# Kernel tuning notes

Hardware: AMD Instinct MI355X
Metric: run time of the kernel (lower is better)

## Reference

```python
import jax, jax.numpy as jnp
import numpy as np

T, H, I, E, Z = 1024, 2048, 1024, 8, 8  # tokens, hidden, moe_intermediate, routed experts, zero experts
TOP_K = 4
ROUTED_SCALING = 1.0


def setup_inputs() -> dict:
    key = jax.random.key(0)
    k0, k1, k2, k3, k4 = jax.random.split(key, 5)
    s = 0.02
    return {
        "hidden_states": jax.random.normal(k0, (T, H), dtype=jnp.float32),
        "router_w": jax.random.normal(k1, (E + Z, H), dtype=jnp.float32) * s,   # classifier weight
        "corr_bias": jnp.zeros((E + Z,), dtype=jnp.float32),                     # e_score_correction_bias
        "w_gate": jax.random.normal(k2, (E, H, I), dtype=jnp.float32) * s,
        "w_up": jax.random.normal(k3, (E, H, I), dtype=jnp.float32) * s,
        "w_down": jax.random.normal(k4, (E, I, H), dtype=jnp.float32) * s,
    }


def reference(hidden_states, router_w, corr_bias, w_gate, w_up, w_down):
    x = hidden_states  # [T, H]
    # ---- router (float32) ----
    logits = x.astype(jnp.float32) @ router_w.T                 # [T, E+Z]
    scores = jax.nn.softmax(logits, axis=-1)
    sel_scores = scores + corr_bias                             # bias used for selection only
    _, topk_idx = jax.lax.top_k(sel_scores, TOP_K)              # [T, K]
    topk_w = jnp.take_along_axis(scores, topk_idx, axis=-1)     # gating weights (renormalize=False)
    topk_w = topk_w * ROUTED_SCALING

    routed = topk_idx < E                                       # [T, K] real-expert mask
    # dense combine weights per routed expert: [T, E]
    onehot = jax.nn.one_hot(jnp.where(routed, topk_idx, 0), E, dtype=x.dtype)
    route_w = jnp.einsum("tke,tk->te", onehot, topk_w * routed.astype(x.dtype))

    # ---- routed experts: silu-gated MLP per expert ----
    gate = jnp.einsum("th,ehi->eti", x, w_gate)                 # [E, T, I]
    up = jnp.einsum("th,ehi->eti", x, w_up)
    mid = jax.nn.silu(gate) * up
    down = jnp.einsum("eti,eih->eth", mid, w_down)              # [E, T, H]
    out = jnp.einsum("te,eth->th", route_w, down)               # combine

    # ---- zero experts (identity type): weight * hidden_states ----
    zero_w = jnp.sum(topk_w * (~routed).astype(x.dtype), axis=-1)  # [T]
    out = out + zero_w[:, None] * x
    return out.astype(hidden_states.dtype)
```

## Files before the change

kernel.cpp:

```cpp
#include <hip/hip_runtime.h>
#include <hip/hip_bf16.h>
#include <math.h>

constexpr int T   = 1024;
constexpr int H   = 2048;
constexpr int I   = 1024;
constexpr int E   = 8;
constexpr int NEZ = 16;
constexpr int TK  = 4;
constexpr int MTG = 24;

typedef short bf16x8 __attribute__((ext_vector_type(8)));
typedef float f32x4  __attribute__((ext_vector_type(4)));
typedef unsigned short u16;
typedef u16 u16x8 __attribute__((ext_vector_type(8)));

#define SYNC() do { asm volatile("s_waitcnt lgkmcnt(0)" ::: "memory"); \
                    __builtin_amdgcn_s_barrier(); } while (0)

__device__ __forceinline__ u16 bf16rn(float x) {
  unsigned u = __builtin_bit_cast(unsigned, x);
  u = u + 0x7FFFu + ((u >> 16) & 1u);
  return (u16)(u >> 16);
}
__device__ __forceinline__ float bf16tof(u16 h) {
  return __builtin_bit_cast(float, (unsigned)h << 16);
}

__global__ __launch_bounds__(256) void prep_a_kernel(
    const float* __restrict__ x, const int* __restrict__ cnt,
    const int* __restrict__ list, u16* __restrict__ Axh, u16* __restrict__ Axl)
{
  const int kt = blockIdx.x;
  const int e  = blockIdx.y;
  int ce = cnt[e]; if (ce > MTG * 16) ce = MTG * 16;
  if (ce == 0) return;
  const int tid = threadIdx.x;
  const int w = tid >> 6, lane = tid & 63;
  const int l15 = lane & 15, lg = lane >> 4;

  for (int mtg = w; mtg < MTG; mtg += 4) {
    int r = mtg * 16 + l15; if (r >= ce) r = ce - 1;
    const int tok = list[e * T + r] >> 2;
    const float* src = x + (size_t)tok * H + kt * 32 + lg * 8;
    const float4 v0 = *(const float4*)(src);
    const float4 v1 = *(const float4*)(src + 4);
    const float vv[8] = {v0.x, v0.y, v0.z, v0.w, v1.x, v1.y, v1.z, v1.w};
    u16x8 h8, l8;
#pragma unroll
    for (int j = 0; j < 8; j++) {
      const u16 hh = bf16rn(vv[j]);
      h8[j] = hh;
      l8[j] = bf16rn(vv[j] - bf16tof(hh));
    }
    const size_t off = (((size_t)e * 64 + kt) * MTG + mtg) * 512 + (size_t)lane * 8;
    *(u16x8*)(Axh + off) = h8;
    *(u16x8*)(Axl + off) = l8;
  }
}

__global__ __launch_bounds__(256) void router_kernel(
    const float* __restrict__ x, const float* __restrict__ rw,
    const float* __restrict__ bias, int* __restrict__ cnt,
    int* __restrict__ list, float* __restrict__ wk4,
    float* __restrict__ zerow)
{
  const int t   = blockIdx.x;
  const int tid = threadIdx.x;
  const float* xt = x + (size_t)t * H;

  float acc[NEZ];
#pragma unroll
  for (int e = 0; e < NEZ; e++) acc[e] = 0.f;

  for (int h = tid; h < H; h += 256) {
    const float xv = xt[h];
#pragma unroll
    for (int e = 0; e < NEZ; e++) acc[e] = fmaf(xv, rw[e * H + h], acc[e]);
  }

#pragma unroll
  for (int e = 0; e < NEZ; e++) {
    float v = acc[e];
#pragma unroll
    for (int off = 32; off >= 1; off >>= 1) v += __shfl_down(v, off, 64);
    acc[e] = v;
  }

  __shared__ float red[4][NEZ];
  const int wv = tid >> 6, ln = tid & 63;
  if (ln == 0) {
#pragma unroll
    for (int e = 0; e < NEZ; e++) red[wv][e] = acc[e];
  }
  __syncthreads();

  if (tid == 0) {
    float l[NEZ];
    float mx = -1e30f;
#pragma unroll
    for (int e = 0; e < NEZ; e++) {
      l[e] = red[0][e] + red[1][e] + red[2][e] + red[3][e];
      mx = fmaxf(mx, l[e]);
    }
    float s = 0.f;
#pragma unroll
    for (int e = 0; e < NEZ; e++) { l[e] = expf(l[e] - mx); s += l[e]; }
    const float inv = 1.f / s;
    float sc[NEZ], sel[NEZ];
#pragma unroll
    for (int e = 0; e < NEZ; e++) {
      sc[e]  = l[e] * inv;
      sel[e] = sc[e] + bias[e];
    }
    float zw = 0.f;
#pragma unroll
    for (int k = 0; k < TK; k++) {
      int best = 0; float bv = sel[0];
#pragma unroll
      for (int e = 1; e < NEZ; e++) {
        if (sel[e] > bv) { bv = sel[e]; best = e; }
      }
      sel[best] = -1e30f;
      const float w = sc[best];
      if (best < E) {
        const int pos = atomicAdd(&cnt[best], 1);
        list[best * T + pos] = (t << 2) | k;
        wk4[t * TK + k] = w;
      } else {
        wk4[t * TK + k] = 0.f;
        zw += w;
      }
    }
    zerow[t] = zw;
  }
}

__global__ __launch_bounds__(256) void gateup_kernel(
    const u16* __restrict__ Axh, const u16* __restrict__ Axl,
    const float* __restrict__ wg, const float* __restrict__ wu,
    const int* __restrict__ cnt, const int* __restrict__ list,
    u16* __restrict__ midh, u16* __restrict__ midl)
{
  const int p = blockIdx.x;
  const int L = (p & 7) * 64 + (p >> 3);
  const int e = L >> 6;
  const int rem = L & 63;
  const int nu = rem & 31;
  const int tg = rem >> 5;
  const int n0 = nu * 32;
  int ce = cnt[e]; if (ce > MTG * 16) ce = MTG * 16;
  if (ce == 0) return;
  const int ntiers = (ce + 63) >> 6;
  if (tg == 1 && ntiers <= 4) return;

  __shared__ __align__(16) char ldsB[3][8192];

  const int tid = threadIdx.x;
  const int w = tid >> 6, lane = tid & 63;
  const int l15 = lane & 15, lg = lane >> 4;
  const int tier = tg * 4 + w;
  const bool alive = (tier < ntiers);

  const int mat = tid >> 7;
  const int oct = (tid >> 5) & 3;
  const int nl  = tid & 31;
  const int ntgw = nl >> 4;
  const int Lw   = (nl & 15) | (oct << 4);
  const int foh  = ((mat << 2) | ntgw) * 1024 + Lw * 16;
  const float* wsrc = (mat ? wu : wg) + (size_t)e * H * I +
                      (size_t)(oct * 8) * I + (size_t)(n0 + nl);

  const int mt0 = (tier <= 5) ? tier * 4 : MTG - 4;
  const char* pAh = (const char*)Axh + (((size_t)e * 64) * MTG + mt0) * 1024 + (size_t)lane * 16;
  const char* pAl = (const char*)Axl + (((size_t)e * 64) * MTG + mt0) * 1024 + (size_t)lane * 16;

  f32x4 accg[4][2] = {};
  f32x4 accu[4][2] = {};
  bf16x8 a0[8], a1[8], a2[8];
  float s0[8], s1[8], s2[8];

#define GU_ISSUE(S, KT) do {                                              \
    const float* ps_ = wsrc + (size_t)(KT) * (32 * (size_t)I);            \
    _Pragma("unroll") for (int j = 0; j < 8; j++) S[j] = ps_[(size_t)j * I]; \
  } while (0)

#define GU_ALOAD(A, KT) do {                                              \
    const size_t ka_ = (size_t)(KT) * (MTG * 1024);                       \
    _Pragma("unroll") for (int q = 0; q < 4; q++) {                       \
      A[q]     = *(const bf16x8*)(pAh + ka_ + q * 1024);                  \
      A[4 + q] = *(const bf16x8*)(pAl + ka_ + q * 1024);                  \
    } } while (0)

#define GU_CONVW(S, WB) do {                                              \
    u16x8 h8_, l8_;                                                       \
    _Pragma("unroll") for (int j = 0; j < 8; j++) {                       \
      const u16 hh_ = bf16rn(S[j]);                                       \
      h8_[j] = hh_; l8_[j] = bf16rn(S[j] - bf16tof(hh_)); }               \
    *(u16x8*)(&ldsB[WB][0] + foh) = h8_;                                  \
    *(u16x8*)(&ldsB[WB][0] + foh + 2048) = l8_;                           \
  } while (0)

#define GU_COMP(RB, A) do {                                               \
    const char* bp_ = &ldsB[RB][0];                                       \
    _Pragma("unroll") for (int ntg = 0; ntg < 2; ntg++) {                 \
      const bf16x8 ggh = *(const bf16x8*)(bp_ + ntg * 1024        + lane * 16); \
      const bf16x8 ggl = *(const bf16x8*)(bp_ + ntg * 1024 + 2048 + lane * 16); \
      const bf16x8 guh = *(const bf16x8*)(bp_ + ntg * 1024 + 4096 + lane * 16); \
      const bf16x8 gul = *(const bf16x8*)(bp_ + ntg * 1024 + 6144 + lane * 16); \
      _Pragma("unroll") for (int mi = 0; mi < 4; mi++) {                  \
        accg[mi][ntg] = __builtin_amdgcn_mfma_f32_16x16x32_bf16(A[mi],     ggh, accg[mi][ntg], 0, 0, 0); \
        accg[mi][ntg] = __builtin_amdgcn_mfma_f32_16x16x32_bf16(A[mi],     ggl, accg[mi][ntg], 0, 0, 0); \
        accg[mi][ntg] = __builtin_amdgcn_mfma_f32_16x16x32_bf16(A[4 + mi], ggh, accg[mi][ntg], 0, 0, 0); \
        accu[mi][ntg] = __builtin_amdgcn_mfma_f32_16x16x32_bf16(A[mi],     guh, accu[mi][ntg], 0, 0, 0); \
        accu[mi][ntg] = __builtin_amdgcn_mfma_f32_16x16x32_bf16(A[mi],     gul, accu[mi][ntg], 0, 0, 0); \
        accu[mi][ntg] = __builtin_amdgcn_mfma_f32_16x16x32_bf16(A[4 + mi], guh, accu[mi][ntg], 0, 0, 0); \
      } } } while (0)

#define GU_BODY(K, SI, AU, AN, SC, RB, WB) do {                           \
    const int k_ = (K);                                                   \
    SYNC();                                                               \
    if (k_ + 3 < 64) GU_ISSUE(SI, k_ + 3);                                \
    if (k_ + 1 < 64) GU_ALOAD(AN, k_ + 1);                                \
    if (alive) GU_COMP(RB, AU);                                           \
    if (k_ + 1 < 64) GU_CONVW(SC, WB);                                    \
  } while (0)

  GU_ISSUE(s0, 0); GU_ISSUE(s1, 1); GU_ISSUE(s2, 2);
  GU_ALOAD(a0, 0);
  GU_CONVW(s0, 0);

  for (int kb = 0; kb < 63; kb += 3) {
    GU_BODY(kb,     s0, a0, a1, s1, 0, 1);
    GU_BODY(kb + 1, s1, a1, a2, s2, 1, 2);
    GU_BODY(kb + 2, s2, a2, a0, s0, 2, 0);
  }
  GU_BODY(63, s0, a0, a1, s1, 0, 1);

#undef GU_ISSUE
#undef GU_ALOAD
#undef GU_CONVW
#undef GU_COMP
#undef GU_BODY

#pragma unroll
  for (int mi = 0; mi < 4; mi++) {
#pragma unroll
    for (int rr = 0; rr < 4; rr++) {
      const int m = tier * 64 + mi * 16 + lg * 4 + rr;
      if (m >= ce) continue;
#pragma unroll
      for (int ntg = 0; ntg < 2; ntg++) {
        const int n = n0 + ntg * 16 + l15;
        const float g = accg[mi][ntg][rr];
        const float u = accu[mi][ntg][rr];
        const float mv = (g / (1.f + expf(-g))) * u;
        const u16 hh = bf16rn(mv);
        const size_t off =
            (((size_t)e * 32 + (n >> 5)) * MTG + (m >> 4)) * 512 +
            (size_t)((m & 15) + ((n >> 3) & 3) * 16) * 8 + (n & 7);
        midh[off] = hh;
        midl[off] = bf16rn(mv - bf16tof(hh));
      }
    }
  }
}

__global__ __launch_bounds__(256) void down_kernel(
    const u16* __restrict__ midh, const u16* __restrict__ midl,
    const float* __restrict__ wd,
    const int* __restrict__ cnt, const int* __restrict__ list,
    float* __restrict__ downb)
{
  const int p = blockIdx.x;
  const int L = (p & 7) * 64 + (p >> 3);
  const int e = L >> 6;
  const int rem = L & 63;
  const int nu = rem & 31;
  const int tg = rem >> 5;
  const int n0 = nu * 64;
  int ce = cnt[e]; if (ce > MTG * 16) ce = MTG * 16;
  if (ce == 0) return;
  const int ntiers = (ce + 63) >> 6;
  if (tg == 1 && ntiers <= 4) return;

  __shared__ __align__(16) char ldsB[3][8192];

  const int tid = threadIdx.x;
  const int w = tid >> 6, lane = tid & 63;
  const int l15 = lane & 15, lg = lane >> 4;
  const int tier = tg * 4 + w;
  const bool alive = (tier < ntiers);

  const int oct = tid >> 6;
  const int nl  = tid & 63;
  const int ntgw = nl >> 4;
  const int Lw   = (nl & 15) | (oct << 4);
  const int foh  = ntgw * 1024 + Lw * 16;
  const float* wsrc = wd + (size_t)e * I * H +
                      (size_t)(oct * 8) * H + (size_t)(n0 + nl);

  const int mt0 = (tier <= 5) ? tier * 4 : MTG - 4;
  const char* pAh = (const char*)midh + (((size_t)e * 32) * MTG + mt0) * 1024 + (size_t)lane * 16;
  const char* pAl = (const char*)midl + (((size_t)e * 32) * MTG + mt0) * 1024 + (size_t)lane * 16;

  f32x4 acc[4][4] = {};
  bf16x8 a0[8], a1[8], a2[8];
  float s0[8], s1[8], s2[8];

#define DN_ISSUE(S, KT) do {                                              \
    const float* ps_ = wsrc + (size_t)(KT) * (32 * (size_t)H);            \
    _Pragma("unroll") for (int j = 0; j < 8; j++) S[j] = ps_[(size_t)j * H]; \
  } while (0)

#define DN_ALOAD(A, KT) do {                                              \
    const size_t ka_ = (size_t)(KT) * (MTG * 1024);                       \
    _Pragma("unroll") for (int q = 0; q < 4; q++) {                       \
      A[q]     = *(const bf16x8*)(pAh + ka_ + q * 1024);                  \
      A[4 + q] = *(const bf16x8*)(pAl + ka_ + q * 1024);                  \
    } } while (0)

#define DN_CONVW(S, WB) do {                                              \
    u16x8 h8_, l8_;                                                       \
    _Pragma("unroll") for (int j = 0; j < 8; j++) {                       \
      const u16 hh_ = bf16rn(S[j]);                                       \
      h8_[j] = hh_; l8_[j] = bf16rn(S[j] - bf16tof(hh_)); }               \
    *(u16x8*)(&ldsB[WB][0] + foh) = h8_;                                  \
    *(u16x8*)(&ldsB[WB][0] + foh + 4096) = l8_;                           \
  } while (0)

#define DN_COMP(RB, A) do {                                               \
    const char* bp_ = &ldsB[RB][0];                                       \
    _Pragma("unroll") for (int ntg = 0; ntg < 4; ntg++) {                 \
      const bf16x8 bh = *(const bf16x8*)(bp_ + ntg * 1024        + lane * 16); \
      const bf16x8 bl = *(const bf16x8*)(bp_ + ntg * 1024 + 4096 + lane * 16); \
      _Pragma("unroll") for (int mi = 0; mi < 4; mi++) {                  \
        acc[mi][ntg] = __builtin_amdgcn_mfma_f32_16x16x32_bf16(A[mi],     bh, acc[mi][ntg], 0, 0, 0); \
        acc[mi][ntg] = __builtin_amdgcn_mfma_f32_16x16x32_bf16(A[mi],     bl, acc[mi][ntg], 0, 0, 0); \
        acc[mi][ntg] = __builtin_amdgcn_mfma_f32_16x16x32_bf16(A[4 + mi], bh, acc[mi][ntg], 0, 0, 0); \
      } } } while (0)

#define DN_BODY(K, SI, AU, AN, SC, RB, WB) do {                           \
    const int k_ = (K);                                                   \
    SYNC();                                                               \
    if (k_ + 3 < 32) DN_ISSUE(SI, k_ + 3);                                \
    if (k_ + 1 < 32) DN_ALOAD(AN, k_ + 1);                                \
    if (alive) DN_COMP(RB, AU);                                           \
    if (k_ + 1 < 32) DN_CONVW(SC, WB);                                    \
  } while (0)

  DN_ISSUE(s0, 0); DN_ISSUE(s1, 1); DN_ISSUE(s2, 2);
  DN_ALOAD(a0, 0);
  DN_CONVW(s0, 0);

  for (int kb = 0; kb < 30; kb += 3) {
    DN_BODY(kb,     s0, a0, a1, s1, 0, 1);
    DN_BODY(kb + 1, s1, a1, a2, s2, 1, 2);
    DN_BODY(kb + 2, s2, a2, a0, s0, 2, 0);
  }
  DN_BODY(30, s0, a0, a1, s1, 0, 1);
  DN_BODY(31, s1, a1, a2, s2, 1, 2);

#undef DN_ISSUE
#undef DN_ALOAD
#undef DN_CONVW
#undef DN_COMP
#undef DN_BODY

#pragma unroll
  for (int mi = 0; mi < 4; mi++) {
#pragma unroll
    for (int rr = 0; rr < 4; rr++) {
      const int m = tier * 64 + mi * 16 + lg * 4 + rr;
      if (m >= ce) continue;
      const int ent  = list[e * T + m];
      const int tok  = ent >> 2;
      const int slot = ent & 3;
      float* drow = downb + ((size_t)tok * TK + slot) * H;
#pragma unroll
      for (int ntg = 0; ntg < 4; ntg++) {
        const int n = n0 + ntg * 16 + l15;
        drow[n] = acc[mi][ntg][rr];
      }
    }
  }
}

__global__ __launch_bounds__(256) void combine_kernel(
    const float* __restrict__ x, const float* __restrict__ downb,
    const float* __restrict__ wk4, const float* __restrict__ zerow,
    float* __restrict__ out)
{
  const int idx = blockIdx.x * 256 + threadIdx.x;
  const int t   = idx >> 9;
  const int h   = (idx & 511) * 4;

  const float w0 = wk4[t * TK + 0];
  const float w1 = wk4[t * TK + 1];
  const float w2 = wk4[t * TK + 2];
  const float w3 = wk4[t * TK + 3];
  const float zw = zerow[t];

  const float4 xv = *(const float4*)(x + (size_t)t * H + h);
  const float4 d0 = *(const float4*)(downb + ((size_t)t * TK + 0) * H + h);
  const float4 d1 = *(const float4*)(downb + ((size_t)t * TK + 1) * H + h);
  const float4 d2 = *(const float4*)(downb + ((size_t)t * TK + 2) * H + h);
  const float4 d3 = *(const float4*)(downb + ((size_t)t * TK + 3) * H + h);

  float4 o;
  o.x = w0 * d0.x + w1 * d1.x + w2 * d2.x + w3 * d3.x + zw * xv.x;
  o.y = w0 * d0.y + w1 * d1.y + w2 * d2.y + w3 * d3.y + zw * xv.y;
  o.z = w0 * d0.z + w1 * d1.z + w2 * d2.z + w3 * d3.z + zw * xv.z;
  o.w = w0 * d0.w + w1 * d1.w + w2 * d2.w + w3 * d3.w + zw * xv.w;
  *(float4*)(out + (size_t)t * H + h) = o;
}

extern "C" void kernel_launch(void* const* d_in, const int* in_sizes, int n_in,
                              void* d_out, int out_size, void* d_ws, size_t ws_size,
                              hipStream_t stream) {
  const float* x    = (const float*)d_in[0];
  const float* rw   = (const float*)d_in[1];
  const float* bias = (const float*)d_in[2];
  const float* wg   = (const float*)d_in[3];
  const float* wu   = (const float*)d_in[4];
  const float* wd   = (const float*)d_in[5];
  float* out = (float*)d_out;

  char* ws = (char*)d_ws;
  size_t off = 0;
  auto alloc = [&](size_t bytes) {
    void* p = ws + off;
    off = (off + bytes + 1023) & ~(size_t)1023;
    return p;
  };
  int*   cnt   = (int*)  alloc(E * sizeof(int));
  int*   list  = (int*)  alloc((size_t)E * T * sizeof(int));
  float* wk4   = (float*)alloc((size_t)T * TK * sizeof(float));
  float* zerow = (float*)alloc((size_t)T * sizeof(float));
  const size_t AXSZ = (size_t)E * 64 * MTG * 512;
  u16*   Axh   = (u16*)  alloc(AXSZ * sizeof(u16));
  u16*   Axl   = (u16*)  alloc(AXSZ * sizeof(u16));
  const size_t MIDSZ = (size_t)E * 32 * MTG * 512;
  u16*   midh  = (u16*)  alloc(MIDSZ * sizeof(u16));
  u16*   midl  = (u16*)  alloc(MIDSZ * sizeof(u16));
  float* downb = (float*)alloc((size_t)T * TK * H * sizeof(float));
  (void)ws_size;

  hipMemsetAsync(cnt, 0, E * sizeof(int), stream);

  router_kernel<<<T, 256, 0, stream>>>(x, rw, bias, cnt, list, wk4, zerow);
  prep_a_kernel<<<dim3(64, 8), 256, 0, stream>>>(x, cnt, list, Axh, Axl);

  gateup_kernel<<<512, 256, 0, stream>>>(
      Axh, Axl, wg, wu, cnt, list, midh, midl);

  down_kernel<<<512, 256, 0, stream>>>(
      midh, midl, wd, cnt, list, downb);

  combine_kernel<<<(T * H / 4) / 256, 256, 0, stream>>>(
      x, downb, wk4, zerow, out);
}
```

Before: 199.0 us.

## Split expert GEMMs into 128-thread blocks covering two M-tiers each

Both the gate/up and down kernels drop from 256-thread blocks covering four 64-row tiers to 128-thread blocks covering two tiers. The grids grow from 512 to 768 blocks, so M-tier groups are spread more finely and fewer waves sit idle when an expert has few tokens. Each thread now loads and converts twice as many weight elements per k-step to fill the same LDS tile. The trade-off is that each weight tile is reloaded and split into bf16 hi/lo by more blocks, which adds global weight traffic and conversion work, and each thread holds more registers.

Result: slower. 209.3 us (+5.2%).

```diff
diff --git a/kernel.cpp b/kernel.cpp
--- a/kernel.cpp
+++ b/kernel.cpp
@@ -136,40 +136,37 @@
   }
 }
 
-__global__ __launch_bounds__(256) void gateup_kernel(
+__global__ __launch_bounds__(128) void gateup_kernel(
     const u16* __restrict__ Axh, const u16* __restrict__ Axl,
     const float* __restrict__ wg, const float* __restrict__ wu,
     const int* __restrict__ cnt, const int* __restrict__ list,
     u16* __restrict__ midh, u16* __restrict__ midl)
 {
   const int p = blockIdx.x;
-  const int L = (p & 7) * 64 + (p >> 3);
-  const int e = L >> 6;
-  const int rem = L & 63;
-  const int nu = rem & 31;
-  const int tg = rem >> 5;
+  const int e = p & 7;
+  const int q = p >> 3;
+  const int nu = q / 3, mg = q % 3;
   const int n0 = nu * 32;
   int ce = cnt[e]; if (ce > MTG * 16) ce = MTG * 16;
   if (ce == 0) return;
   const int ntiers = (ce + 63) >> 6;
-  if (tg == 1 && ntiers <= 4) return;
+  if (mg * 2 >= ntiers) return;
 
   __shared__ __align__(16) char ldsB[3][8192];
 
   const int tid = threadIdx.x;
   const int w = tid >> 6, lane = tid & 63;
   const int l15 = lane & 15, lg = lane >> 4;
-  const int tier = tg * 4 + w;
+  const int tier = mg * 2 + w;
   const bool alive = (tier < ntiers);
 
-  const int mat = tid >> 7;
   const int oct = (tid >> 5) & 3;
   const int nl  = tid & 31;
   const int ntgw = nl >> 4;
   const int Lw   = (nl & 15) | (oct << 4);
-  const int foh  = ((mat << 2) | ntgw) * 1024 + Lw * 16;
-  const float* wsrc = (mat ? wu : wg) + (size_t)e * H * I +
-                      (size_t)(oct * 8) * I + (size_t)(n0 + nl);
+  const int fohG = ntgw * 1024 + Lw * 16;
+  const float* wsG = wg + (size_t)e * H * I + (size_t)(oct * 8) * I + (size_t)(n0 + nl);
+  const float* wsU = wu + (size_t)e * H * I + (size_t)(oct * 8) * I + (size_t)(n0 + nl);
 
   const int mt0 = (tier <= 5) ? tier * 4 : MTG - 4;
   const char* pAh = (const char*)Axh + (((size_t)e * 64) * MTG + mt0) * 1024 + (size_t)lane * 16;
@@ -178,27 +175,36 @@
   f32x4 accg[4][2] = {};
   f32x4 accu[4][2] = {};
   bf16x8 a0[8], a1[8], a2[8];
-  float s0[8], s1[8], s2[8];
+  float s0[16], s1[16], s2[16];
+
+  constexpr int NB = 64;
 
 #define GU_ISSUE(S, KT) do {                                              \
-    const float* ps_ = wsrc + (size_t)(KT) * (32 * (size_t)I);            \
-    _Pragma("unroll") for (int j = 0; j < 8; j++) S[j] = ps_[(size_t)j * I]; \
-  } while (0)
+    const float* pg_ = wsG + (size_t)(KT) * (32 * (size_t)I);             \
+    const float* pu_ = wsU + (size_t)(KT) * (32 * (size_t)I);             \
+    _Pragma("unroll") for (int j = 0; j < 8; j++) {                       \
+      S[j]     = pg_[(size_t)j * I];                                      \
+      S[8 + j] = pu_[(size_t)j * I];                                      \
+    } } while (0)
 
 #define GU_ALOAD(A, KT) do {                                              \
     const size_t ka_ = (size_t)(KT) * (MTG * 1024);                       \
-    _Pragma("unroll") for (int q = 0; q < 4; q++) {                       \
-      A[q]     = *(const bf16x8*)(pAh + ka_ + q * 1024);                  \
-      A[4 + q] = *(const bf16x8*)(pAl + ka_ + q * 1024);                  \
+    _Pragma("unroll") for (int qn = 0; qn < 4; qn++) {                    \
+      A[qn]     = *(const bf16x8*)(pAh + ka_ + qn * 1024);                \
+      A[4 + qn] = *(const bf16x8*)(pAl + ka_ + qn * 1024);                \
     } } while (0)
 
 #define GU_CONVW(S, WB) do {                                              \
-    u16x8 h8_, l8_;                                                       \
+    u16x8 gh_, gl_, uh_, ul_;                                             \
     _Pragma("unroll") for (int j = 0; j < 8; j++) {                       \
-      const u16 hh_ = bf16rn(S[j]);                                       \
-      h8_[j] = hh_; l8_[j] = bf16rn(S[j] - bf16tof(hh_)); }               \
-    *(u16x8*)(&ldsB[WB][0] + foh) = h8_;                                  \
-    *(u16x8*)(&ldsB[WB][0] + foh + 2048) = l8_;                           \
+      const u16 h1_ = bf16rn(S[j]);                                       \
+      gh_[j] = h1_; gl_[j] = bf16rn(S[j] - bf16tof(h1_));                 \
+      const u16 h2_ = bf16rn(S[8 + j]);                                   \
+      uh_[j] = h2_; ul_[j] = bf16rn(S[8 + j] - bf16tof(h2_)); }           \
+    *(u16x8*)(&ldsB[WB][0] + fohG)        = gh_;                          \
+    *(u16x8*)(&ldsB[WB][0] + fohG + 2048) = gl_;                          \
+    *(u16x8*)(&ldsB[WB][0] + fohG + 4096) = uh_;                          \
+    *(u16x8*)(&ldsB[WB][0] + fohG + 6144) = ul_;                          \
   } while (0)
 
 #define GU_COMP(RB, A) do {                                               \
@@ -220,10 +226,10 @@
 #define GU_BODY(K, SI, AU, AN, SC, RB, WB) do {                           \
     const int k_ = (K);                                                   \
     SYNC();                                                               \
-    if (k_ + 3 < 64) GU_ISSUE(SI, k_ + 3);                                \
-    if (k_ + 1 < 64) GU_ALOAD(AN, k_ + 1);                                \
+    if (k_ + 3 < NB) GU_ISSUE(SI, k_ + 3);                                \
+    if (k_ + 1 < NB) GU_ALOAD(AN, k_ + 1);                                \
     if (alive) GU_COMP(RB, AU);                                           \
-    if (k_ + 1 < 64) GU_CONVW(SC, WB);                                    \
+    if (k_ + 1 < NB) GU_CONVW(SC, WB);                                    \
   } while (0)
 
   GU_ISSUE(s0, 0); GU_ISSUE(s1, 1); GU_ISSUE(s2, 2);
@@ -243,62 +249,62 @@
 #undef GU_COMP
 #undef GU_BODY
 
-#pragma unroll
-  for (int mi = 0; mi < 4; mi++) {
-#pragma unroll
-    for (int rr = 0; rr < 4; rr++) {
-      const int m = tier * 64 + mi * 16 + lg * 4 + rr;
-      if (m >= ce) continue;
-#pragma unroll
-      for (int ntg = 0; ntg < 2; ntg++) {
-        const int n = n0 + ntg * 16 + l15;
-        const float g = accg[mi][ntg][rr];
-        const float u = accu[mi][ntg][rr];
-        const float mv = (g / (1.f + expf(-g))) * u;
-        const u16 hh = bf16rn(mv);
-        const size_t off =
-            (((size_t)e * 32 + (n >> 5)) * MTG + (m >> 4)) * 512 +
-            (size_t)((m & 15) + ((n >> 3) & 3) * 16) * 8 + (n & 7);
-        midh[off] = hh;
-        midl[off] = bf16rn(mv - bf16tof(hh));
+  if (alive) {
+#pragma unroll
+    for (int mi = 0; mi < 4; mi++) {
+#pragma unroll
+      for (int rr = 0; rr < 4; rr++) {
+        const int m = tier * 64 + mi * 16 + lg * 4 + rr;
+        if (m >= ce) continue;
+#pragma unroll
+        for (int ntg = 0; ntg < 2; ntg++) {
+          const int n = n0 + ntg * 16 + l15;
+          const float g = accg[mi][ntg][rr];
+          const float u = accu[mi][ntg][rr];
+          const float mv = (g / (1.f + expf(-g))) * u;
+          const u16 hh = bf16rn(mv);
+          const size_t off =
+              (((size_t)e * 32 + (n >> 5)) * MTG + (m >> 4)) * 512 +
+              (size_t)((m & 15) + ((n >> 3) & 3) * 16) * 8 + (n & 7);
+          midh[off] = hh;
+          midl[off] = bf16rn(mv - bf16tof(hh));
+        }
       }
     }
   }
 }
 
-__global__ __launch_bounds__(256) void down_kernel(
+__global__ __launch_bounds__(128) void down_kernel(
     const u16* __restrict__ midh, const u16* __restrict__ midl,
     const float* __restrict__ wd,
     const int* __restrict__ cnt, const int* __restrict__ list,
     float* __restrict__ downb)
 {
   const int p = blockIdx.x;
-  const int L = (p & 7) * 64 + (p >> 3);
-  const int e = L >> 6;
-  const int rem = L & 63;
-  const int nu = rem & 31;
-  const int tg = rem >> 5;
+  const int e = p & 7;
+  const int q = p >> 3;
+  const int nu = q / 3, mg = q % 3;
   const int n0 = nu * 64;
   int ce = cnt[e]; if (ce > MTG * 16) ce = MTG * 16;
   if (ce == 0) return;
   const int ntiers = (ce + 63) >> 6;
-  if (tg == 1 && ntiers <= 4) return;
+  if (mg * 2 >= ntiers) return;
 
   __shared__ __align__(16) char ldsB[3][8192];
 
   const int tid = threadIdx.x;
   const int w = tid >> 6, lane = tid & 63;
   const int l15 = lane & 15, lg = lane >> 4;
-  const int tier = tg * 4 + w;
+  const int tier = mg * 2 + w;
   const bool alive = (tier < ntiers);
 
-  const int oct = tid >> 6;
-  const int nl  = tid & 63;
-  const int ntgw = nl >> 4;
-  const int Lw   = (nl & 15) | (oct << 4);
-  const int foh  = ntgw * 1024 + Lw * 16;
-  const float* wsrc = wd + (size_t)e * I * H +
-                      (size_t)(oct * 8) * H + (size_t)(n0 + nl);
+  const int oct = (tid >> 5) & 3;
+  const int nl0 = tid & 31;
+  const int Lw  = (nl0 & 15) | (oct << 4);
+  const int foh0 = (nl0 >> 4) * 1024 + Lw * 16;
+  const int foh1 = ((nl0 + 32) >> 4) * 1024 + Lw * 16;
+  const float* ws0 = wd + (size_t)e * I * H + (size_t)(oct * 8) * H + (size_t)(n0 + nl0);
+  const float* ws1 = ws0 + 32;
 
   const int mt0 = (tier <= 5) ? tier * 4 : MTG - 4;
   const char* pAh = (const char*)midh + (((size_t)e * 32) * MTG + mt0) * 1024 + (size_t)lane * 16;
@@ -306,27 +312,36 @@
 
   f32x4 acc[4][4] = {};
   bf16x8 a0[8], a1[8], a2[8];
-  float s0[8], s1[8], s2[8];
+  float s0[16], s1[16], s2[16];
+
+  constexpr int NB = 32;
 
 #define DN_ISSUE(S, KT) do {                                              \
-    const float* ps_ = wsrc + (size_t)(KT) * (32 * (size_t)H);            \
-    _Pragma("unroll") for (int j = 0; j < 8; j++) S[j] = ps_[(size_t)j * H]; \
-  } while (0)
+    const float* p0_ = ws0 + (size_t)(KT) * (32 * (size_t)H);             \
+    const float* p1_ = ws1 + (size_t)(KT) * (32 * (size_t)H);             \
+    _Pragma("unroll") for (int j = 0; j < 8; j++) {                       \
+      S[j]     = p0_[(size_t)j * H];                                      \
+      S[8 + j] = p1_[(size_t)j * H];                                      \
+    } } while (0)
 
 #define DN_ALOAD(A, KT) do {                                              \
     const size_t ka_ = (size_t)(KT) * (MTG * 1024);                       \
-    _Pragma("unroll") for (int q = 0; q < 4; q++) {                       \
-      A[q]     = *(const bf16x8*)(pAh + ka_ + q * 1024);                  \
-      A[4 + q] = *(const bf16x8*)(pAl + ka_ + q * 1024);                  \
+    _Pragma("unroll") for (int qn = 0; qn < 4; qn++) {                    \
+      A[qn]     = *(const bf16x8*)(pAh + ka_ + qn * 1024);                \
+      A[4 + qn] = *(const bf16x8*)(pAl + ka_ + qn * 1024);                \
     } } while (0)
 
 #define DN_CONVW(S, WB) do {                                              \
-    u16x8 h8_, l8_;                                                       \
+    u16x8 h0_, l0_, h1_, l1_;                                             \
     _Pragma("unroll") for (int j = 0; j < 8; j++) {                       \
-      const u16 hh_ = bf16rn(S[j]);                                       \
-      h8_[j] = hh_; l8_[j] = bf16rn(S[j] - bf16tof(hh_)); }               \
-    *(u16x8*)(&ldsB[WB][0] + foh) = h8_;                                  \
-    *(u16x8*)(&ldsB[WB][0] + foh + 4096) = l8_;                           \
+      const u16 a_ = bf16rn(S[j]);                                        \
+      h0_[j] = a_; l0_[j] = bf16rn(S[j] - bf16tof(a_));                   \
+      const u16 b_ = bf16rn(S[8 + j]);                                    \
+      h1_[j] = b_; l1_[j] = bf16rn(S[8 + j] - bf16tof(b_)); }             \
+    *(u16x8*)(&ldsB[WB][0] + foh0)        = h0_;                          \
+    *(u16x8*)(&ldsB[WB][0] + foh0 + 4096) = l0_;                          \
+    *(u16x8*)(&ldsB[WB][0] + foh1)        = h1_;                          \
+    *(u16x8*)(&ldsB[WB][0] + foh1 + 4096) = l1_;                          \
   } while (0)
 
 #define DN_COMP(RB, A) do {                                               \
@@ -343,10 +358,10 @@
 #define DN_BODY(K, SI, AU, AN, SC, RB, WB) do {                           \
     const int k_ = (K);                                                   \
     SYNC();                                                               \
-    if (k_ + 3 < 32) DN_ISSUE(SI, k_ + 3);                                \
-    if (k_ + 1 < 32) DN_ALOAD(AN, k_ + 1);                                \
+    if (k_ + 3 < NB) DN_ISSUE(SI, k_ + 3);                                \
+    if (k_ + 1 < NB) DN_ALOAD(AN, k_ + 1);                                \
     if (alive) DN_COMP(RB, AU);                                           \
-    if (k_ + 1 < 32) DN_CONVW(SC, WB);                                    \
+    if (k_ + 1 < NB) DN_CONVW(SC, WB);                                    \
   } while (0)
 
   DN_ISSUE(s0, 0); DN_ISSUE(s1, 1); DN_ISSUE(s2, 2);
@@ -367,20 +382,22 @@
 #undef DN_COMP
 #undef DN_BODY
 
-#pragma unroll
-  for (int mi = 0; mi < 4; mi++) {
-#pragma unroll
-    for (int rr = 0; rr < 4; rr++) {
-      const int m = tier * 64 + mi * 16 + lg * 4 + rr;
-      if (m >= ce) continue;
-      const int ent  = list[e * T + m];
-      const int tok  = ent >> 2;
-      const int slot = ent & 3;
-      float* drow = downb + ((size_t)tok * TK + slot) * H;
-#pragma unroll
-      for (int ntg = 0; ntg < 4; ntg++) {
-        const int n = n0 + ntg * 16 + l15;
-        drow[n] = acc[mi][ntg][rr];
+  if (alive) {
+#pragma unroll
+    for (int mi = 0; mi < 4; mi++) {
+#pragma unroll
+      for (int rr = 0; rr < 4; rr++) {
+        const int m = tier * 64 + mi * 16 + lg * 4 + rr;
+        if (m >= ce) continue;
+        const int ent  = list[e * T + m];
+        const int tok  = ent >> 2;
+        const int slot = ent & 3;
+        float* drow = downb + ((size_t)tok * TK + slot) * H;
+#pragma unroll
+        for (int ntg = 0; ntg < 4; ntg++) {
+          const int n = n0 + ntg * 16 + l15;
+          drow[n] = acc[mi][ntg][rr];
+        }
       }
     }
   }
@@ -451,10 +468,10 @@
   router_kernel<<<T, 256, 0, stream>>>(x, rw, bias, cnt, list, wk4, zerow);
   prep_a_kernel<<<dim3(64, 8), 256, 0, stream>>>(x, cnt, list, Axh, Axl);
 
-  gateup_kernel<<<512, 256, 0, stream>>>(
+  gateup_kernel<<<768, 128, 0, stream>>>(
       Axh, Axl, wg, wu, cnt, list, midh, midl);
 
-  down_kernel<<<512, 256, 0, stream>>>(
+  down_kernel<<<768, 128, 0, stream>>>(
       midh, midl, wd, cnt, list, downb);
 
   combine_kernel<<<(T * H / 4) / 256, 256, 0, stream>>>(
```

## Load expert weights directly into registers per wave, dropping LDS staging

Applied to the files above, without the earlier changes.

Both the gate/up and down GEMM kernels no longer stage fp32 weights through a triple-buffered LDS ring with block barriers. Each wave now loads its own B fragments straight from global memory into registers, splits them into bf16 hi/lo, and runs a two-deep register double buffer. Waves with no token tier exit early instead of idling at barriers. The cost is that each wave reloads the same weight tile independently, multiplying global/L2 weight traffic by up to four per block, and register pressure rises with the 16- or 32-float staging arrays.

Measured after the change: 257.1 us. 1.29x slower.

```diff
diff --git a/kernel.cpp b/kernel.cpp
--- a/kernel.cpp
+++ b/kernel.cpp
@@ -14,9 +14,6 @@
 typedef float f32x4  __attribute__((ext_vector_type(4)));
 typedef unsigned short u16;
 typedef u16 u16x8 __attribute__((ext_vector_type(8)));
-
-#define SYNC() do { asm volatile("s_waitcnt lgkmcnt(0)" ::: "memory"); \
-                    __builtin_amdgcn_s_barrier(); } while (0)
 
 __device__ __forceinline__ u16 bf16rn(float x) {
   unsigned u = __builtin_bit_cast(unsigned, x);
@@ -146,102 +143,79 @@
   const int L = (p & 7) * 64 + (p >> 3);
   const int e = L >> 6;
   const int rem = L & 63;
-  const int nu = rem & 31;
+  const int n0 = (rem & 31) * 32;
   const int tg = rem >> 5;
-  const int n0 = nu * 32;
   int ce = cnt[e]; if (ce > MTG * 16) ce = MTG * 16;
   if (ce == 0) return;
   const int ntiers = (ce + 63) >> 6;
-  if (tg == 1 && ntiers <= 4) return;
-
-  __shared__ __align__(16) char ldsB[3][8192];
 
   const int tid = threadIdx.x;
   const int w = tid >> 6, lane = tid & 63;
   const int l15 = lane & 15, lg = lane >> 4;
+
   const int tier = tg * 4 + w;
-  const bool alive = (tier < ntiers);
-
-  const int mat = tid >> 7;
-  const int oct = (tid >> 5) & 3;
-  const int nl  = tid & 31;
-  const int ntgw = nl >> 4;
-  const int Lw   = (nl & 15) | (oct << 4);
-  const int foh  = ((mat << 2) | ntgw) * 1024 + Lw * 16;
-  const float* wsrc = (mat ? wu : wg) + (size_t)e * H * I +
-                      (size_t)(oct * 8) * I + (size_t)(n0 + nl);
-
-  const int mt0 = (tier <= 5) ? tier * 4 : MTG - 4;
-  const char* pAh = (const char*)Axh + (((size_t)e * 64) * MTG + mt0) * 1024 + (size_t)lane * 16;
-  const char* pAl = (const char*)Axl + (((size_t)e * 64) * MTG + mt0) * 1024 + (size_t)lane * 16;
+  if (tier >= ntiers) return;
+
+  const float* pG0 = wg + (size_t)e * H * I + (size_t)(lg * 8) * I + (n0 + l15);
+  const float* pG1 = pG0 + 16;
+  const float* pU0 = wu + (size_t)e * H * I + (size_t)(lg * 8) * I + (n0 + l15);
+  const float* pU1 = pU0 + 16;
+
+  const size_t ao = (((size_t)e * 64) * MTG + (size_t)tier * 4) * 1024 + (size_t)lane * 16;
+  const char* pAh = (const char*)Axh + ao;
+  const char* pAl = (const char*)Axl + ao;
 
   f32x4 accg[4][2] = {};
   f32x4 accu[4][2] = {};
-  bf16x8 a0[8], a1[8], a2[8];
-  float s0[8], s1[8], s2[8];
-
-#define GU_ISSUE(S, KT) do {                                              \
-    const float* ps_ = wsrc + (size_t)(KT) * (32 * (size_t)I);            \
-    _Pragma("unroll") for (int j = 0; j < 8; j++) S[j] = ps_[(size_t)j * I]; \
-  } while (0)
-
-#define GU_ALOAD(A, KT) do {                                              \
+
+  bf16x8 A0[8], A1[8];
+  float sG0[16], sU0[16], sG1[16], sU1[16];
+
+  constexpr int NB = 64;
+
+#define GU_LOAD(SG, SU, A, KT) do {                                       \
+    const size_t kb_ = (size_t)(KT) * (32 * (size_t)I);                   \
+    _Pragma("unroll") for (int j = 0; j < 8; j++) {                       \
+      SG[j]     = pG0[kb_ + (size_t)j * I];                               \
+      SG[8 + j] = pG1[kb_ + (size_t)j * I];                               \
+      SU[j]     = pU0[kb_ + (size_t)j * I];                               \
+      SU[8 + j] = pU1[kb_ + (size_t)j * I];                               \
+    }                                                                     \
     const size_t ka_ = (size_t)(KT) * (MTG * 1024);                       \
     _Pragma("unroll") for (int q = 0; q < 4; q++) {                       \
       A[q]     = *(const bf16x8*)(pAh + ka_ + q * 1024);                  \
       A[4 + q] = *(const bf16x8*)(pAl + ka_ + q * 1024);                  \
     } } while (0)
 
-#define GU_CONVW(S, WB) do {                                              \
-    u16x8 h8_, l8_;                                                       \
-    _Pragma("unroll") for (int j = 0; j < 8; j++) {                       \
-      const u16 hh_ = bf16rn(S[j]);                                       \
-      h8_[j] = hh_; l8_[j] = bf16rn(S[j] - bf16tof(hh_)); }               \
-    *(u16x8*)(&ldsB[WB][0] + foh) = h8_;                                  \
-    *(u16x8*)(&ldsB[WB][0] + foh + 2048) = l8_;                           \
-  } while (0)
-
-#define GU_COMP(RB, A) do {                                               \
-    const char* bp_ = &ldsB[RB][0];                                       \
+#define GU_STEP(SG, SU, A) do {                                           \
     _Pragma("unroll") for (int ntg = 0; ntg < 2; ntg++) {                 \
-      const bf16x8 ggh = *(const bf16x8*)(bp_ + ntg * 1024        + lane * 16); \
-      const bf16x8 ggl = *(const bf16x8*)(bp_ + ntg * 1024 + 2048 + lane * 16); \
-      const bf16x8 guh = *(const bf16x8*)(bp_ + ntg * 1024 + 4096 + lane * 16); \
-      const bf16x8 gul = *(const bf16x8*)(bp_ + ntg * 1024 + 6144 + lane * 16); \
+      bf16x8 gh_, gl_, uh_, ul_;                                          \
+      _Pragma("unroll") for (int j = 0; j < 8; j++) {                     \
+        const float gv_ = SG[ntg * 8 + j];                                \
+        const u16 g1_ = bf16rn(gv_);                                      \
+        gh_[j] = (short)g1_; gl_[j] = (short)bf16rn(gv_ - bf16tof(g1_));  \
+        const float uv_ = SU[ntg * 8 + j];                                \
+        const u16 u1_ = bf16rn(uv_);                                      \
+        uh_[j] = (short)u1_; ul_[j] = (short)bf16rn(uv_ - bf16tof(u1_));  \
+      }                                                                   \
       _Pragma("unroll") for (int mi = 0; mi < 4; mi++) {                  \
-        accg[mi][ntg] = __builtin_amdgcn_mfma_f32_16x16x32_bf16(A[mi],     ggh, accg[mi][ntg], 0, 0, 0); \
-        accg[mi][ntg] = __builtin_amdgcn_mfma_f32_16x16x32_bf16(A[mi],     ggl, accg[mi][ntg], 0, 0, 0); \
-        accg[mi][ntg] = __builtin_amdgcn_mfma_f32_16x16x32_bf16(A[4 + mi], ggh, accg[mi][ntg], 0, 0, 0); \
-        accu[mi][ntg] = __builtin_amdgcn_mfma_f32_16x16x32_bf16(A[mi],     guh, accu[mi][ntg], 0, 0, 0); \
-        accu[mi][ntg] = __builtin_amdgcn_mfma_f32_16x16x32_bf16(A[mi],     gul, accu[mi][ntg], 0, 0, 0); \
-        accu[mi][ntg] = __builtin_amdgcn_mfma_f32_16x16x32_bf16(A[4 + mi], guh, accu[mi][ntg], 0, 0, 0); \
+        accg[mi][ntg] = __builtin_amdgcn_mfma_f32_16x16x32_bf16(A[mi],     gh_, accg[mi][ntg], 0, 0, 0); \
+        accg[mi][ntg] = __builtin_amdgcn_mfma_f32_16x16x32_bf16(A[mi],     gl_, accg[mi][ntg], 0, 0, 0); \
+        accg[mi][ntg] = __builtin_amdgcn_mfma_f32_16x16x32_bf16(A[4 + mi], gh_, accg[mi][ntg], 0, 0, 0); \
+        accu[mi][ntg] = __builtin_amdgcn_mfma_f32_16x16x32_bf16(A[mi],     uh_, accu[mi][ntg], 0, 0, 0); \
+        accu[mi][ntg] = __builtin_amdgcn_mfma_f32_16x16x32_bf16(A[mi],     ul_, accu[mi][ntg], 0, 0, 0); \
+        accu[mi][ntg] = __builtin_amdgcn_mfma_f32_16x16x32_bf16(A[4 + mi], uh_, accu[mi][ntg], 0, 0, 0); \
       } } } while (0)
 
-#define GU_BODY(K, SI, AU, AN, SC, RB, WB) do {                           \
-    const int k_ = (K);                                                   \
-    SYNC();                                                               \
-    if (k_ + 3 < 64) GU_ISSUE(SI, k_ + 3);                                \
-    if (k_ + 1 < 64) GU_ALOAD(AN, k_ + 1);                                \
-    if (alive) GU_COMP(RB, AU);                                           \
-    if (k_ + 1 < 64) GU_CONVW(SC, WB);                                    \
-  } while (0)
-
-  GU_ISSUE(s0, 0); GU_ISSUE(s1, 1); GU_ISSUE(s2, 2);
-  GU_ALOAD(a0, 0);
-  GU_CONVW(s0, 0);
-
-  for (int kb = 0; kb < 63; kb += 3) {
-    GU_BODY(kb,     s0, a0, a1, s1, 0, 1);
-    GU_BODY(kb + 1, s1, a1, a2, s2, 1, 2);
-    GU_BODY(kb + 2, s2, a2, a0, s0, 2, 0);
-  }
-  GU_BODY(63, s0, a0, a1, s1, 0, 1);
-
-#undef GU_ISSUE
-#undef GU_ALOAD
-#undef GU_CONVW
-#undef GU_COMP
-#undef GU_BODY
+  GU_LOAD(sG0, sU0, A0, 0);
+  for (int t = 0; t < NB; t += 2) {
+    GU_LOAD(sG1, sU1, A1, t + 1);
+    GU_STEP(sG0, sU0, A0);
+    if (t + 2 < NB) GU_LOAD(sG0, sU0, A0, t + 2);
+    GU_STEP(sG1, sU1, A1);
+  }
+#undef GU_LOAD
+#undef GU_STEP
 
 #pragma unroll
   for (int mi = 0; mi < 4; mi++) {
@@ -276,96 +250,72 @@
   const int L = (p & 7) * 64 + (p >> 3);
   const int e = L >> 6;
   const int rem = L & 63;
-  const int nu = rem & 31;
+  const int n0 = (rem & 31) * 64;
   const int tg = rem >> 5;
-  const int n0 = nu * 64;
   int ce = cnt[e]; if (ce > MTG * 16) ce = MTG * 16;
   if (ce == 0) return;
   const int ntiers = (ce + 63) >> 6;
-  if (tg == 1 && ntiers <= 4) return;
-
-  __shared__ __align__(16) char ldsB[3][8192];
 
   const int tid = threadIdx.x;
   const int w = tid >> 6, lane = tid & 63;
   const int l15 = lane & 15, lg = lane >> 4;
+
   const int tier = tg * 4 + w;
-  const bool alive = (tier < ntiers);
-
-  const int oct = tid >> 6;
-  const int nl  = tid & 63;
-  const int ntgw = nl >> 4;
-  const int Lw   = (nl & 15) | (oct << 4);
-  const int foh  = ntgw * 1024 + Lw * 16;
-  const float* wsrc = wd + (size_t)e * I * H +
-                      (size_t)(oct * 8) * H + (size_t)(n0 + nl);
-
-  const int mt0 = (tier <= 5) ? tier * 4 : MTG - 4;
-  const char* pAh = (const char*)midh + (((size_t)e * 32) * MTG + mt0) * 1024 + (size_t)lane * 16;
-  const char* pAl = (const char*)midl + (((size_t)e * 32) * MTG + mt0) * 1024 + (size_t)lane * 16;
+  if (tier >= ntiers) return;
+
+  const float* pB0 = wd + (size_t)e * I * H + (size_t)(lg * 8) * H + (n0 + l15);
+  const float* pB1 = pB0 + 16;
+  const float* pB2 = pB0 + 32;
+  const float* pB3 = pB0 + 48;
+
+  const size_t ao = (((size_t)e * 32) * MTG + (size_t)tier * 4) * 1024 + (size_t)lane * 16;
+  const char* pAh = (const char*)midh + ao;
+  const char* pAl = (const char*)midl + ao;
 
   f32x4 acc[4][4] = {};
-  bf16x8 a0[8], a1[8], a2[8];
-  float s0[8], s1[8], s2[8];
-
-#define DN_ISSUE(S, KT) do {                                              \
-    const float* ps_ = wsrc + (size_t)(KT) * (32 * (size_t)H);            \
-    _Pragma("unroll") for (int j = 0; j < 8; j++) S[j] = ps_[(size_t)j * H]; \
-  } while (0)
-
-#define DN_ALOAD(A, KT) do {                                              \
+
+  bf16x8 A0[8], A1[8];
+  float sB0[32], sB1[32];
+
+  constexpr int NB = 32;
+
+#define DN_LOAD(SB, A, KT) do {                                           \
+    const size_t kb_ = (size_t)(KT) * (32 * (size_t)H);                   \
+    _Pragma("unroll") for (int j = 0; j < 8; j++) {                       \
+      SB[j]      = pB0[kb_ + (size_t)j * H];                              \
+      SB[8 + j]  = pB1[kb_ + (size_t)j * H];                              \
+      SB[16 + j] = pB2[kb_ + (size_t)j * H];                              \
+      SB[24 + j] = pB3[kb_ + (size_t)j * H];                              \
+    }                                                                     \
     const size_t ka_ = (size_t)(KT) * (MTG * 1024);                       \
     _Pragma("unroll") for (int q = 0; q < 4; q++) {                       \
       A[q]     = *(const bf16x8*)(pAh + ka_ + q * 1024);                  \
       A[4 + q] = *(const bf16x8*)(pAl + ka_ + q * 1024);                  \
     } } while (0)
 
-#define DN_CONVW(S, WB) do {                                              \
-    u16x8 h8_, l8_;                                                       \
-    _Pragma("unroll") for (int j = 0; j < 8; j++) {                       \
-      const u16 hh_ = bf16rn(S[j]);                                       \
-      h8_[j] = hh_; l8_[j] = bf16rn(S[j] - bf16tof(hh_)); }               \
-    *(u16x8*)(&ldsB[WB][0] + foh) = h8_;                                  \
-    *(u16x8*)(&ldsB[WB][0] + foh + 4096) = l8_;                           \
-  } while (0)
-
-#define DN_COMP(RB, A) do {                                               \
-    const char* bp_ = &ldsB[RB][0];                                       \
+#define DN_STEP(SB, A) do {                                               \
     _Pragma("unroll") for (int ntg = 0; ntg < 4; ntg++) {                 \
-      const bf16x8 bh = *(const bf16x8*)(bp_ + ntg * 1024        + lane * 16); \
-      const bf16x8 bl = *(const bf16x8*)(bp_ + ntg * 1024 + 4096 + lane * 16); \
+      bf16x8 bh_, bl_;                                                    \
+      _Pragma("unroll") for (int j = 0; j < 8; j++) {                     \
+        const float bv_ = SB[ntg * 8 + j];                                \
+        const u16 b1_ = bf16rn(bv_);                                      \
+        bh_[j] = (short)b1_; bl_[j] = (short)bf16rn(bv_ - bf16tof(b1_));  \
+      }                                                                   \
       _Pragma("unroll") for (int mi = 0; mi < 4; mi++) {                  \
-        acc[mi][ntg] = __builtin_amdgcn_mfma_f32_16x16x32_bf16(A[mi],     bh, acc[mi][ntg], 0, 0, 0); \
-        acc[mi][ntg] = __builtin_amdgcn_mfma_f32_16x16x32_bf16(A[mi],     bl, acc[mi][ntg], 0, 0, 0); \
-        acc[mi][ntg] = __builtin_amdgcn_mfma_f32_16x16x32_bf16(A[4 + mi], bh, acc[mi][ntg], 0, 0, 0); \
+        acc[mi][ntg] = __builtin_amdgcn_mfma_f32_16x16x32_bf16(A[mi],     bh_, acc[mi][ntg], 0, 0, 0); \
+        acc[mi][ntg] = __builtin_amdgcn_mfma_f32_16x16x32_bf16(A[mi],     bl_, acc[mi][ntg], 0, 0, 0); \
+        acc[mi][ntg] = __builtin_amdgcn_mfma_f32_16x16x32_bf16(A[4 + mi], bh_, acc[mi][ntg], 0, 0, 0); \
       } } } while (0)
 
-#define DN_BODY(K, SI, AU, AN, SC, RB, WB) do {                           \
-    const int k_ = (K);                                                   \
-    SYNC();                                                               \
-    if (k_ + 3 < 32) DN_ISSUE(SI, k_ + 3);                                \
-    if (k_ + 1 < 32) DN_ALOAD(AN, k_ + 1);                                \
-    if (alive) DN_COMP(RB, AU);                                           \
-    if (k_ + 1 < 32) DN_CONVW(SC, WB);                                    \
-  } while (0)
-
-  DN_ISSUE(s0, 0); DN_ISSUE(s1, 1); DN_ISSUE(s2, 2);
-  DN_ALOAD(a0, 0);
-  DN_CONVW(s0, 0);
-
-  for (int kb = 0; kb < 30; kb += 3) {
-    DN_BODY(kb,     s0, a0, a1, s1, 0, 1);
-    DN_BODY(kb + 1, s1, a1, a2, s2, 1, 2);
-    DN_BODY(kb + 2, s2, a2, a0, s0, 2, 0);
-  }
-  DN_BODY(30, s0, a0, a1, s1, 0, 1);
-  DN_BODY(31, s1, a1, a2, s2, 1, 2);
-
-#undef DN_ISSUE
-#undef DN_ALOAD
-#undef DN_CONVW
-#undef DN_COMP
-#undef DN_BODY
+  DN_LOAD(sB0, A0, 0);
+  for (int t = 0; t < NB; t += 2) {
+    DN_LOAD(sB1, A1, t + 1);
+    DN_STEP(sB0, A0);
+    if (t + 2 < NB) DN_LOAD(sB0, A0, t + 2);
+    DN_STEP(sB1, A1);
+  }
+#undef DN_LOAD
+#undef DN_STEP
 
 #pragma unroll
   for (int mi = 0; mi < 4; mi++) {
```
